# Kernel optimization log

Measured on AMD Instinct MI355X. Metric: run time of the kernel, lower is better.

## Reference

```python
import jax, jax.numpy as jnp
import numpy as np
from jax.scipy.special import erf

N, M = 2048, 32


def setup_inputs() -> dict:
    key = jax.random.key(0)
    k1, k2, k3, k4 = jax.random.split(key, 4)
    predicted_risk = jax.random.normal(k1, (N, M), dtype=jnp.float32)
    expressions = jax.random.normal(k2, (N, M), dtype=jnp.float32)
    predicted_tr = jax.random.normal(k3, (N, M), dtype=jnp.float32)
    event_indicator = (jax.random.uniform(k4, (N, M)) < 0.3).astype(jnp.float32)
    sigma = jnp.float32(1.0)
    return {
        "predicted_risk": predicted_risk,
        "expressions": expressions,
        "predicted_tr": predicted_tr,
        "event_indicator": event_indicator,
        "sigma": sigma,
    }


def reference(predicted_risk, expressions, predicted_tr, event_indicator, sigma):
    # time_indicator: (n, m), normalized per-feature and scaled by 2*sigma*sqrt(2)
    ti = jnp.exp(expressions - predicted_tr)
    ti = ti / jnp.max(ti, axis=0) / (2.0 * sigma * jnp.sqrt(jnp.float32(2.0)))
    n, m = expressions.shape
    # location[j, a, k] = ti[j, k] - ti[a, k]   -> (n, n, m)
    location = ti[:, None, :] - ti[None, :, :]
    phi = 0.5 * (1.0 + erf(-location))
    # diagonal correction: phi[i, i, :] += 0.5
    idx = jnp.arange(n)
    phi = phi.at[idx, idx].add(0.5)
    # cumsum^T[j, k] = sum_a exp(predicted_risk[a, k]) * phi[j, a, k]
    expH = jnp.exp(predicted_risk)  # (n, m)
    log_cumsum = jnp.log(jnp.einsum('am,jam->jm', expH, phi))  # (n, m)
    sum_loglik = jnp.sum((predicted_risk - log_cumsum) * event_indicator)
    return -sum_loglik
```

## Files before the change

kernel.cpp:

```cpp
#include <hip/hip_runtime.h>
#include <math.h>

#define NROWS 2048
#define MCOLS 32

#define C1 1.1283791671f
#define C3 (-0.3761263890f)
#define C5 0.1128379167f
#define C7 (-0.0268661706f)

__global__ __launch_bounds__(256) void k_init(float* __restrict__ Mp,
                                              unsigned int* __restrict__ maxbits,
                                              float* __restrict__ out) {
    int t = threadIdx.x;
    Mp[t] = 0.0f;
    if (t < MCOLS) maxbits[t] = 0u;
    if (t == 0) out[0] = 0.0f;
}

__global__ __launch_bounds__(256) void k_elem(const float* __restrict__ expr,
                                              const float* __restrict__ tr,
                                              const float* __restrict__ risk,
                                              float* __restrict__ ws_t,
                                              float* __restrict__ ws_e,
                                              float* __restrict__ Mp,
                                              unsigned int* __restrict__ maxbits) {
    int tid = threadIdx.x;
    int i = blockIdx.x * 256 + tid;
    float tv = __expf(expr[i] - tr[i]);
    float ev = __expf(risk[i]);
    ws_t[i] = tv;
    ws_e[i] = ev;

    __shared__ float sm_t[256];
    __shared__ float sm_e[256];
    sm_t[tid] = tv; sm_e[tid] = ev;
    __syncthreads();

    int k = tid & 31;
    int q = tid >> 5;
    float partial = 0.0f, mx = 0.0f;
#pragma unroll
    for (int r = 0; r < 8; r++) {
        float t = sm_t[r * 32 + k];
        float e = sm_e[r * 32 + k];
        float p = e;
        for (int m = 0; m < q; m++) p *= t;
        partial += p;
        mx = fmaxf(mx, t);
    }
    atomicAdd(&Mp[q * 32 + k], partial);
    if (q == 0) atomicMax(&maxbits[k], __float_as_uint(mx));
}

__global__ __launch_bounds__(64) void k_coeff(const float* __restrict__ Mp,
                                              const unsigned int* __restrict__ maxbits,
                                              const float* __restrict__ sigma,
                                              float* __restrict__ D,
                                              float* __restrict__ scaleS,
                                              float* __restrict__ Shalf) {
    int k = threadIdx.x;
    if (k >= MCOLS) return;
    float s = 1.0f / (__uint_as_float(maxbits[k]) * 2.0f * sigma[0] * sqrtf(2.0f));
    float M[8];
    float sp = 1.0f;
#pragma unroll
    for (int q = 0; q < 8; q++) { M[q] = Mp[q * 32 + k] * sp; sp *= s; }
    D[0 * 32 + k] = C1 * M[1] +         C3 * M[3] +         C5 * M[5] +        C7 * M[7];
    D[1 * 32 + k] = C1 * M[0] + 3.0f *  C3 * M[2] + 5.0f *  C5 * M[4] + 7.0f * C7 * M[6];
    D[2 * 32 + k] = 3.0f * C3 * M[1] + 10.0f * C5 * M[3] + 21.0f * C7 * M[5];
    D[3 * 32 + k] = C3 * M[0] + 10.0f * C5 * M[2] + 35.0f * C7 * M[4];
    D[4 * 32 + k] = 5.0f * C5 * M[1] + 35.0f * C7 * M[3];
    D[5 * 32 + k] = C5 * M[0] + 21.0f * C7 * M[2];
    D[6 * 32 + k] = 7.0f * C7 * M[1];
    D[7 * 32 + k] = C7 * M[0];
    scaleS[k] = s;
    Shalf[k]  = 0.5f * M[0];
}

__global__ __launch_bounds__(256) void k_final(const float* __restrict__ ws_t,
                                               const float* __restrict__ ws_e,
                                               const float* __restrict__ D,
                                               const float* __restrict__ scaleS,
                                               const float* __restrict__ Shalf,
                                               const float* __restrict__ risk,
                                               const float* __restrict__ event,
                                               float* __restrict__ out) {
    int tid = threadIdx.x;
    int i = blockIdx.x * 256 + tid;
    __shared__ float sD[256];
    __shared__ float sSc[32];
    __shared__ float sSh[32];
    __shared__ float warpsum[4];
    sD[tid] = D[tid];
    if (tid < 32) { sSc[tid] = scaleS[tid]; sSh[tid] = Shalf[tid]; }
    __syncthreads();

    int k = i & 31;
    float w = -(ws_t[i] * sSc[k]);
    float acc = sD[7 * 32 + k];
#pragma unroll
    for (int q = 6; q >= 0; q--)
        acc = fmaf(acc, w, sD[q * 32 + k]);
    float cum = sSh[k] + 0.5f * (acc + ws_e[i]);
    float c = (__logf(cum) - risk[i]) * event[i];

    for (int off = 32; off > 0; off >>= 1)
        c += __shfl_down(c, off, 64);
    if ((tid & 63) == 0) warpsum[tid >> 6] = c;
    __syncthreads();
    if (tid == 0) {
        float s = (warpsum[0] + warpsum[1]) + (warpsum[2] + warpsum[3]);
        atomicAdd(out, s);
    }
}

extern "C" void kernel_launch(void* const* d_in, const int* in_sizes, int n_in,
                              void* d_out, int out_size, void* d_ws, size_t ws_size,
                              hipStream_t stream) {
    const float* risk  = (const float*)d_in[0];
    const float* expr  = (const float*)d_in[1];
    const float* tr    = (const float*)d_in[2];
    const float* event = (const float*)d_in[3];
    const float* sigma = (const float*)d_in[4];
    float* out = (float*)d_out;

    float*        ws_t    = (float*)d_ws;
    float*        ws_e    = ws_t + NROWS * MCOLS;
    float*        ws_Mp   = ws_e + NROWS * MCOLS;
    float*        ws_D    = ws_Mp + 8 * MCOLS;
    float*        ws_sc   = ws_D + 8 * MCOLS;
    float*        ws_Sh   = ws_sc + MCOLS;
    unsigned int* ws_max  = (unsigned int*)(ws_Sh + MCOLS);

    k_init<<<1, 256, 0, stream>>>(ws_Mp, ws_max, out);
    k_elem<<<(NROWS * MCOLS) / 256, 256, 0, stream>>>(expr, tr, risk, ws_t, ws_e,
                                                      ws_Mp, ws_max);
    k_coeff<<<1, 64, 0, stream>>>(ws_Mp, ws_max, sigma, ws_D, ws_sc, ws_Sh);
    k_final<<<(NROWS * MCOLS) / 256, 256, 0, stream>>>(ws_t, ws_e, ws_D, ws_sc,
                                                       ws_Sh, risk, event, out);
}
```

Measured before the change: 76.25 us.

## Fuse four launches into two with deterministic partials and float4 loads

The init and coefficient kernels are removed. The first kernel now writes per-block moment partials and per-block column maxima, with no atomics. Each block of the loss kernel redundantly reduces those 64 partials, builds the polynomial coefficients in shared memory, and recomputes the exponentials from the raw inputs instead of reading stored intermediates. Loads are float4 and the grid shrinks to 64 blocks, which cuts launch overhead and global traffic at the cost of redundant per-block reduction work and fewer blocks in flight.

```diff
diff --git a/kernel.cpp b/kernel.cpp
--- a/kernel.cpp
+++ b/kernel.cpp
@@ -9,101 +9,115 @@
 #define C5 0.1128379167f
 #define C7 (-0.0268661706f)
 
-__global__ __launch_bounds__(256) void k_init(float* __restrict__ Mp,
-                                              unsigned int* __restrict__ maxbits,
-                                              float* __restrict__ out) {
-    int t = threadIdx.x;
-    Mp[t] = 0.0f;
-    if (t < MCOLS) maxbits[t] = 0u;
-    if (t == 0) out[0] = 0.0f;
-}
+__global__ __launch_bounds__(256) void k_moments(const float4* __restrict__ expr4,
+                                                 const float4* __restrict__ tr4,
+                                                 const float4* __restrict__ risk4,
+                                                 float* __restrict__ partial,
+                                                 float* __restrict__ pmax,
+                                                 float* __restrict__ out) {
+    int tid = threadIdx.x, b = blockIdx.x;
+    int i4 = b * 256 + tid;
 
-__global__ __launch_bounds__(256) void k_elem(const float* __restrict__ expr,
-                                              const float* __restrict__ tr,
-                                              const float* __restrict__ risk,
-                                              float* __restrict__ ws_t,
-                                              float* __restrict__ ws_e,
-                                              float* __restrict__ Mp,
-                                              unsigned int* __restrict__ maxbits) {
-    int tid = threadIdx.x;
-    int i = blockIdx.x * 256 + tid;
-    float tv = __expf(expr[i] - tr[i]);
-    float ev = __expf(risk[i]);
-    ws_t[i] = tv;
-    ws_e[i] = ev;
+    float4 ex = expr4[i4];
+    float4 tv = tr4[i4];
+    float4 rk = risk4[i4];
 
-    __shared__ float sm_t[256];
-    __shared__ float sm_e[256];
-    sm_t[tid] = tv; sm_e[tid] = ev;
+    __shared__ float sm_t[1024];
+    __shared__ float sm_e[1024];
+    float4 t4 = make_float4(__expf(ex.x - tv.x), __expf(ex.y - tv.y),
+                            __expf(ex.z - tv.z), __expf(ex.w - tv.w));
+    float4 e4 = make_float4(__expf(rk.x), __expf(rk.y),
+                            __expf(rk.z), __expf(rk.w));
+    ((float4*)sm_t)[tid] = t4;
+    ((float4*)sm_e)[tid] = e4;
     __syncthreads();
 
+    int q = tid >> 5;
     int k = tid & 31;
-    int q = tid >> 5;
-    float partial = 0.0f, mx = 0.0f;
+    float part = 0.0f, mx = 0.0f;
 #pragma unroll
-    for (int r = 0; r < 8; r++) {
+    for (int r = 0; r < 32; r++) {
         float t = sm_t[r * 32 + k];
         float e = sm_e[r * 32 + k];
         float p = e;
+#pragma unroll 7
         for (int m = 0; m < q; m++) p *= t;
-        partial += p;
+        part += p;
         mx = fmaxf(mx, t);
     }
-    atomicAdd(&Mp[q * 32 + k], partial);
-    if (q == 0) atomicMax(&maxbits[k], __float_as_uint(mx));
+    partial[b * 256 + tid] = part;
+    if (q == 0) pmax[b * 32 + k] = mx;
+    if (b == 0 && tid == 0) out[0] = 0.0f;
 }
 
-__global__ __launch_bounds__(64) void k_coeff(const float* __restrict__ Mp,
-                                              const unsigned int* __restrict__ maxbits,
+__global__ __launch_bounds__(256) void k_loss(const float4* __restrict__ expr4,
+                                              const float4* __restrict__ tr4,
+                                              const float4* __restrict__ risk4,
+                                              const float4* __restrict__ event4,
                                               const float* __restrict__ sigma,
-                                              float* __restrict__ D,
-                                              float* __restrict__ scaleS,
-                                              float* __restrict__ Shalf) {
-    int k = threadIdx.x;
-    if (k >= MCOLS) return;
-    float s = 1.0f / (__uint_as_float(maxbits[k]) * 2.0f * sigma[0] * sqrtf(2.0f));
-    float M[8];
-    float sp = 1.0f;
-#pragma unroll
-    for (int q = 0; q < 8; q++) { M[q] = Mp[q * 32 + k] * sp; sp *= s; }
-    D[0 * 32 + k] = C1 * M[1] +         C3 * M[3] +         C5 * M[5] +        C7 * M[7];
-    D[1 * 32 + k] = C1 * M[0] + 3.0f *  C3 * M[2] + 5.0f *  C5 * M[4] + 7.0f * C7 * M[6];
-    D[2 * 32 + k] = 3.0f * C3 * M[1] + 10.0f * C5 * M[3] + 21.0f * C7 * M[5];
-    D[3 * 32 + k] = C3 * M[0] + 10.0f * C5 * M[2] + 35.0f * C7 * M[4];
-    D[4 * 32 + k] = 5.0f * C5 * M[1] + 35.0f * C7 * M[3];
-    D[5 * 32 + k] = C5 * M[0] + 21.0f * C7 * M[2];
-    D[6 * 32 + k] = 7.0f * C7 * M[1];
-    D[7 * 32 + k] = C7 * M[0];
-    scaleS[k] = s;
-    Shalf[k]  = 0.5f * M[0];
-}
-
-__global__ __launch_bounds__(256) void k_final(const float* __restrict__ ws_t,
-                                               const float* __restrict__ ws_e,
-                                               const float* __restrict__ D,
-                                               const float* __restrict__ scaleS,
-                                               const float* __restrict__ Shalf,
-                                               const float* __restrict__ risk,
-                                               const float* __restrict__ event,
-                                               float* __restrict__ out) {
+                                              const float* __restrict__ partial,
+                                              const float* __restrict__ pmax,
+                                              float* __restrict__ out) {
     int tid = threadIdx.x;
-    int i = blockIdx.x * 256 + tid;
+    __shared__ float sM[256];
+    __shared__ float sMax[32];
     __shared__ float sD[256];
     __shared__ float sSc[32];
     __shared__ float sSh[32];
     __shared__ float warpsum[4];
-    sD[tid] = D[tid];
-    if (tid < 32) { sSc[tid] = scaleS[tid]; sSh[tid] = Shalf[tid]; }
+
+    float acc = 0.0f;
+    for (int bb = 0; bb < 64; bb++) acc += partial[bb * 256 + tid];
+    sM[tid] = acc;
+    if (tid < 32) {
+        float mx = 0.0f;
+        for (int bb = 0; bb < 64; bb++) mx = fmaxf(mx, pmax[bb * 32 + tid]);
+        sMax[tid] = mx;
+    }
     __syncthreads();
 
-    int k = i & 31;
-    float w = -(ws_t[i] * sSc[k]);
-    float acc = sD[7 * 32 + k];
+    if (tid < 32) {
+        int k = tid;
+        float s = 1.0f / (sMax[k] * 2.0f * sigma[0] * sqrtf(2.0f));
+        float M[8];
+        float sp = 1.0f;
 #pragma unroll
-    for (int q = 6; q >= 0; q--)
-        acc = fmaf(acc, w, sD[q * 32 + k]);
-    float cum = sSh[k] + 0.5f * (acc + ws_e[i]);
-    float c = (__logf(cum) - risk[i]) * event[i];
+        for (int q = 0; q < 8; q++) { M[q] = sM[q * 32 + k] * sp; sp *= s; }
+        sD[0 * 32 + k] = C1 * M[1] +         C3 * M[3] +         C5 * M[5] +        C7 * M[7];
+        sD[1 * 32 + k] = C1 * M[0] + 3.0f *  C3 * M[2] + 5.0f *  C5 * M[4] + 7.0f * C7 * M[6];
+        sD[2 * 32 + k] = 3.0f * C3 * M[1] + 10.0f * C5 * M[3] + 21.0f * C7 * M[5];
+        sD[3 * 32 + k] = C3 * M[0] + 10.0f * C5 * M[2] + 35.0f * C7 * M[4];
+        sD[4 * 32 + k] = 5.0f * C5 * M[1] + 35.0f * C7 * M[3];
+        sD[5 * 32 + k] = C5 * M[0] + 21.0f * C7 * M[2];
+        sD[6 * 32 + k] = 7.0f * C7 * M[1];
+        sD[7 * 32 + k] = C7 * M[0];
+        sSc[k] = s;
+        sSh[k] = 0.5f * M[0];
+    }
+    __syncthreads();
+
+    int i4 = blockIdx.x * 256 + tid;
+    float4 ex = expr4[i4];
+    float4 tv = tr4[i4];
+    float4 rk = risk4[i4];
+    float4 ev = event4[i4];
+
+    float c = 0.0f;
+    const float* exp_ = &ex.x; const float* trp = &tv.x;
+    const float* rkp  = &rk.x; const float* evp = &ev.x;
+    int k0 = (tid * 4) & 31;
+#pragma unroll
+    for (int j = 0; j < 4; j++) {
+        int k = k0 + j;
+        float t = __expf(exp_[j] - trp[j]);
+        float e = __expf(rkp[j]);
+        float w = -(t * sSc[k]);
+        float h = sD[7 * 32 + k];
+#pragma unroll
+        for (int q = 6; q >= 0; q--) h = fmaf(h, w, sD[q * 32 + k]);
+        float cum = sSh[k] + 0.5f * (h + e);
+        c += (__logf(cum) - rkp[j]) * evp[j];
+    }
 
     for (int off = 32; off > 0; off >>= 1)
         c += __shfl_down(c, off, 64);
@@ -118,25 +132,17 @@
 extern "C" void kernel_launch(void* const* d_in, const int* in_sizes, int n_in,
                               void* d_out, int out_size, void* d_ws, size_t ws_size,
                               hipStream_t stream) {
-    const float* risk  = (const float*)d_in[0];
-    const float* expr  = (const float*)d_in[1];
-    const float* tr    = (const float*)d_in[2];
-    const float* event = (const float*)d_in[3];
-    const float* sigma = (const float*)d_in[4];
+    const float4* risk  = (const float4*)d_in[0];
+    const float4* expr  = (const float4*)d_in[1];
+    const float4* tr    = (const float4*)d_in[2];
+    const float4* event = (const float4*)d_in[3];
+    const float*  sigma = (const float*)d_in[4];
     float* out = (float*)d_out;
 
-    float*        ws_t    = (float*)d_ws;
-    float*        ws_e    = ws_t + NROWS * MCOLS;
-    float*        ws_Mp   = ws_e + NROWS * MCOLS;
-    float*        ws_D    = ws_Mp + 8 * MCOLS;
-    float*        ws_sc   = ws_D + 8 * MCOLS;
-    float*        ws_Sh   = ws_sc + MCOLS;
-    unsigned int* ws_max  = (unsigned int*)(ws_Sh + MCOLS);
+    float* ws_partial = (float*)d_ws;
+    float* ws_pmax    = ws_partial + 64 * 256;
 
-    k_init<<<1, 256, 0, stream>>>(ws_Mp, ws_max, out);
-    k_elem<<<(NROWS * MCOLS) / 256, 256, 0, stream>>>(expr, tr, risk, ws_t, ws_e,
-                                                      ws_Mp, ws_max);
-    k_coeff<<<1, 64, 0, stream>>>(ws_Mp, ws_max, sigma, ws_D, ws_sc, ws_Sh);
-    k_final<<<(NROWS * MCOLS) / 256, 256, 0, stream>>>(ws_t, ws_e, ws_D, ws_sc,
-                                                       ws_Sh, risk, event, out);
+    k_moments<<<64, 256, 0, stream>>>(expr, tr, risk, ws_partial, ws_pmax, out);
+    k_loss<<<64, 256, 0, stream>>>(expr, tr, risk, event, sigma,
+                                   ws_partial, ws_pmax, out);
 }
```

Result: slower. 84.72 us (+11.1%).
